# Optimization experiments

Measured on AMD Instinct MI355X. Metric: run time of the kernel, lower is better.

Reference implementation:

```python
import jax, jax.numpy as jnp
import numpy as np

NUM_HEADS = 16


def setup_inputs() -> dict:
    key = jax.random.key(0)
    ks = jax.random.split(key, 5)
    B, S, D = 2, 2048, 1024
    scale = 0.02
    return {
        "x": jax.random.normal(ks[0], (B, S, D), dtype=jnp.float32),
        "Wq": jax.random.normal(ks[1], (D, D), dtype=jnp.float32) * scale,
        "Wk": jax.random.normal(ks[2], (D, D), dtype=jnp.float32) * scale,
        "Wv": jax.random.normal(ks[3], (D, D), dtype=jnp.float32) * scale,
        "Wo": jax.random.normal(ks[4], (D, D), dtype=jnp.float32) * scale,
        "bo": jnp.zeros((D,), dtype=jnp.float32),
    }


def reference(x, Wq, Wk, Wv, Wo, bo):
    B, S, D = x.shape
    H = NUM_HEADS
    Dh = D // H
    # project and split heads -> [B, H, S, Dh]
    q = (x @ Wq).reshape(B, S, H, Dh).transpose(0, 2, 1, 3)
    k = (x @ Wk).reshape(B, S, H, Dh).transpose(0, 2, 1, 3)
    v = (x @ Wv).reshape(B, S, H, Dh).transpose(0, 2, 1, 3)
    # full causal attention scores [B, H, S, S]
    scores = jnp.einsum("bhqd,bhkd->bhqk", q, k)
    causal_mask = jnp.triu(jnp.ones((S, S), dtype=bool), k=1)
    scores = jnp.where(causal_mask, -jnp.inf, scores)
    attn = jax.nn.softmax(scores / jnp.sqrt(jnp.float32(Dh)), axis=-1)
    ctx = jnp.einsum("bhqk,bhkd->bhqd", attn, v)
    ctx = ctx.transpose(0, 2, 1, 3).reshape(B, S, D)
    return ctx @ Wo + bo
```

## Files before the change

kernel.cpp:

```cpp
#include <hip/hip_runtime.h>
#include <hip/hip_bf16.h>
#include <math.h>

typedef __bf16 bf16_t;
typedef bf16_t bf16x4 __attribute__((ext_vector_type(4)));
typedef bf16_t bf16x8 __attribute__((ext_vector_type(8)));
typedef float f32x4 __attribute__((ext_vector_type(4)));

#define MFMA16(a, b, c) __builtin_amdgcn_mfma_f32_16x16x32_bf16(a, b, c, 0, 0, 0)
#define NEG_BIG (-1e30f)
#define QSCALE 0.18033688f

#define GLL16(gp, lp)                                                          \
    __builtin_amdgcn_global_load_lds(                                          \
        (const __attribute__((address_space(1))) unsigned int*)(gp),           \
        (__attribute__((address_space(3))) unsigned int*)(lp), 16, 0, 0)


__global__ __launch_bounds__(256) void prep(const float* __restrict__ x,
                                            const float* __restrict__ Wq,
                                            const float* __restrict__ Wk,
                                            const float* __restrict__ Wv,
                                            const float* __restrict__ Wo,
                                            bf16_t* __restrict__ Xb,
                                            bf16_t* __restrict__ WTqkv,
                                            bf16_t* __restrict__ WoT) {
    __shared__ float tile[32][33];
    const int z = blockIdx.z;
    const int tx = threadIdx.x, ty = threadIdx.y;
    if (z == 4) {
        int i0 = (((blockIdx.y * 32 + blockIdx.x) * 256) + ty * 32 + tx) * 4;
        for (int j = 0; j < 4; j++) {
            int i = i0 + j * 1048576;
            float4 v = *(const float4*)(x + i);
            Xb[i + 0] = (bf16_t)v.x;
            Xb[i + 1] = (bf16_t)v.y;
            Xb[i + 2] = (bf16_t)v.z;
            Xb[i + 3] = (bf16_t)v.w;
        }
    } else {
        const float* W = (z == 0) ? Wq : (z == 1) ? Wk : (z == 2) ? Wv : Wo;
        bf16_t* WT = (z < 3) ? (WTqkv + (size_t)z * 1048576) : WoT;
        int bx = blockIdx.x * 32, by = blockIdx.y * 32;
        for (int i = 0; i < 32; i += 8)
            tile[ty + i][tx] = W[(size_t)(by + ty + i) * 1024 + bx + tx];
        __syncthreads();
        for (int i = 0; i < 32; i += 8)
            WT[(size_t)(bx + ty + i) * 1024 + by + tx] = (bf16_t)tile[tx][ty + i];
    }
}

__global__ __launch_bounds__(256) void gemm_qkv(const bf16_t* __restrict__ X,
                                                const bf16_t* __restrict__ WT,
                                                bf16_t* __restrict__ Qd,
                                                bf16_t* __restrict__ Kd,
                                                bf16_t* __restrict__ Vd) {
    __shared__ bf16_t AsmF[128 * 64];
    __shared__ bf16_t BsmF[128 * 64];
    const int which = blockIdx.z;
    const bf16_t* Wt = WT + (size_t)which * 1024 * 1024;
    const int bm = blockIdx.y * 128;
    const int bn = blockIdx.x * 128;
    const int tid = threadIdx.x;
    const int wave = tid >> 6, lane = tid & 63;
    const int wm = (wave >> 1) * 64, wn = (wave & 1) * 64;
    const int col = lane & 15, quad = lane >> 4;
    const int cswz = col & 7;
    const int lr8 = lane >> 3;
    const int jg = (lane & 7) ^ lr8;

    const int srow = wave * 32 + lr8;
    const bf16_t* gA = X  + (size_t)(bm + srow) * 1024 + jg * 8;
    const bf16_t* gB = Wt + (size_t)(bn + srow) * 1024 + jg * 8;
    bf16_t* lA = AsmF + wave * 2048;
    bf16_t* lB = BsmF + wave * 2048;

    f32x4 acc[4][4] = {};

    for (int k0 = 0; k0 < 1024; k0 += 64) {
        for (int j = 0; j < 4; j++) {
            GLL16(gA + (size_t)j * 8192 + k0, lA + j * 512);
            GLL16(gB + (size_t)j * 8192 + k0, lB + j * 512);
        }
        __syncthreads();
        for (int ks = 0; ks < 2; ks++) {
            bf16x8 af[4], bfr[4];
            for (int mi = 0; mi < 4; mi++)
                af[mi] = *(const bf16x8*)&AsmF[(wm + mi * 16 + col) * 64 +
                                               (((ks << 2) + quad) ^ cswz) * 8];
            for (int ni = 0; ni < 4; ni++)
                bfr[ni] = *(const bf16x8*)&BsmF[(wn + ni * 16 + col) * 64 +
                                                (((ks << 2) + quad) ^ cswz) * 8];
            if (which != 2) {
                for (int mi = 0; mi < 4; mi++)
                    for (int ni = 0; ni < 4; ni++)
                        acc[mi][ni] = MFMA16(af[mi], bfr[ni], acc[mi][ni]);
            } else {
                for (int mi = 0; mi < 4; mi++)
                    for (int ni = 0; ni < 4; ni++)
                        acc[mi][ni] = MFMA16(bfr[ni], af[mi], acc[mi][ni]);
            }
        }
        __syncthreads();
    }

    if (which != 2) {
        const float sc = (which == 0) ? QSCALE : 1.0f;
        for (int mi = 0; mi < 4; mi++) {
            for (int ni = 0; ni < 4; ni++) {
                int mbase = bm + wm + mi * 16 + quad * 4;
                int n = bn + wn + ni * 16 + col;
                int h = n >> 6, dh = n & 63;
                for (int r = 0; r < 4; r++) {
                    int m = mbase + r;
                    int b = m >> 11, s = m & 2047;
                    size_t bh = (size_t)b * 16 + h;
                    bf16_t val = (bf16_t)(acc[mi][ni][r] * sc);
                    if (which == 0) Qd[(bh * 2048 + s) * 64 + dh] = val;
                    else            Kd[(bh * 2048 + s) * 64 + dh] = val;
                }
            }
        }
    } else {
        for (int mi = 0; mi < 4; mi++) {
            for (int ni = 0; ni < 4; ni++) {
                int nbase = bn + wn + ni * 16 + quad * 4;
                int m = bm + wm + mi * 16 + col;
                int b = m >> 11, s = m & 2047;
                for (int r = 0; r < 4; r++) {
                    int n = nbase + r;
                    int h = n >> 6, dh = n & 63;
                    size_t bh = (size_t)b * 16 + h;
                    Vd[(bh * 64 + dh) * 2048 + s] = (bf16_t)acc[mi][ni][r];
                }
            }
        }
    }
}

__global__ __launch_bounds__(256) void attn(const bf16_t* __restrict__ Q,
                                            const bf16_t* __restrict__ K,
                                            const bf16_t* __restrict__ VT,
                                            bf16_t* __restrict__ CTX) {
    __shared__ bf16_t KsF[2 * 64 * 64];
    __shared__ bf16_t VsF[2 * 64 * 64];
    __shared__ bf16_t PsF[4 * 16 * 64];

    const int bidx = blockIdx.x;
    const int bh = bidx & 31;
    const int qt = 31 - (bidx >> 5);
    const int tid = threadIdx.x;
    const int wave = tid >> 6, lane = tid & 63;
    const int col = lane & 15, quad = lane >> 4;
    const int cswz = col & 7;
    const int lr8 = lane >> 3;
    const int jg = (lane & 7) ^ lr8;

    const bf16_t* Qb = Q + (size_t)bh * 2048 * 64;
    const bf16_t* Kb = K + (size_t)bh * 2048 * 64;
    const bf16_t* Vb = VT + (size_t)bh * 64 * 2048;

    const int strow = wave * 16 + lr8;
    const bf16_t* gK = Kb + (size_t)strow * 64 + jg * 8;
    const bf16_t* gV = Vb + (size_t)strow * 2048 + jg * 8;

    const int b_ = bh >> 4, h_ = bh & 15;

    bf16x8 ones;
    for (int i = 0; i < 8; i++) ones[i] = (bf16_t)1.0f;

    bf16_t* PsRow = PsF + wave * 1024 + col * 64;

    auto stage = [&](int k0, int bsel) {
        bf16_t* lK = KsF + bsel * 4096 + wave * 1024;
        bf16_t* lV = VsF + bsel * 4096 + wave * 1024;
        for (int j = 0; j < 2; j++) {
            GLL16(gK + (size_t)(k0 + j * 8) * 64, lK + j * 512);
            GLL16(gV + (size_t)(k0 + j * 8 * 2048), lV + j * 512);
        }
    };

    stage(0, 0);

    const int q0 = qt * 64;
    const int qrow = q0 + wave * 16 + col;
    const bf16x8 qf0 = *(const bf16x8*)&Qb[(size_t)qrow * 64 + quad * 8];
    const bf16x8 qf1 = *(const bf16x8*)&Qb[(size_t)qrow * 64 + 32 + quad * 8];

    f32x4 o[4] = {};
    f32x4 accl = {};

    const int nt = qt + 1;
    for (int g = 0; g < nt; g++) {
        __syncthreads();
        if (g + 1 < nt) stage((g + 1) * 64, (g + 1) & 1);

        const int bsel = g & 1;
        const bf16_t* Kbuf = KsF + bsel * 4096;
        const bf16_t* Vbuf = VsF + bsel * 4096;
        const bool diag = (g == qt);

        for (int ksub = 0; ksub < 4; ksub++) {
            bf16x8 a0 = *(const bf16x8*)&Kbuf[(ksub * 16 + col) * 64 +
                                              (quad ^ cswz) * 8];
            bf16x8 a1 = *(const bf16x8*)&Kbuf[(ksub * 16 + col) * 64 +
                                              ((4 + quad) ^ cswz) * 8];
            f32x4 z = {};
            z = MFMA16(a0, qf0, z);
            z = MFMA16(a1, qf1, z);
            if (diag) {
                for (int r = 0; r < 4; r++) {
                    int lk = ksub * 16 + quad * 4 + r;
                    if (lk > wave * 16 + col) z[r] = NEG_BIG;
                }
            }
            bf16x4 pw;
            for (int r = 0; r < 4; r++)
                pw[r] = (bf16_t)exp2f(z[r]);
            *(bf16x4*)&PsRow[((ksub * 2 + (quad >> 1)) ^ cswz) * 8 +
                             (quad & 1) * 4] = pw;
        }

        for (int ck = 0; ck < 2; ck++) {
            bf16x8 pf = *(const bf16x8*)&PsRow[((ck * 4 + quad) ^ cswz) * 8];
            accl = MFMA16(pf, ones, accl);
            for (int d = 0; d < 4; d++) {
                bf16x8 vf = *(const bf16x8*)&Vbuf[(d * 16 + col) * 64 +
                                                  (((ck << 2) + quad) ^ cswz) * 8];
                o[d] = MFMA16(pf, vf, o[d]);
            }
        }
    }

    for (int d = 0; d < 4; d++) {
        for (int r = 0; r < 4; r++) {
            int s = q0 + wave * 16 + quad * 4 + r;
            CTX[((size_t)(b_ * 2048 + s)) * 1024 + h_ * 64 + d * 16 + col] =
                (bf16_t)(o[d][r] / fmaxf(accl[r], 1e-20f));
        }
    }
}

__global__ __launch_bounds__(256) void gemm_out(const bf16_t* __restrict__ X,
                                                const bf16_t* __restrict__ WT,
                                                const float* __restrict__ BO,
                                                float* __restrict__ OUT) {
    __shared__ bf16_t AsmF[64 * 64];
    __shared__ bf16_t BsmF[128 * 64];
    const int bm = blockIdx.y * 64;
    const int bn = blockIdx.x * 128;
    const int tid = threadIdx.x;
    const int wave = tid >> 6, lane = tid & 63;
    const int wm = (wave >> 1) * 32, wn = (wave & 1) * 64;
    const int col = lane & 15, quad = lane >> 4;
    const int cswz = col & 7;
    const int lr8 = lane >> 3;
    const int jg = (lane & 7) ^ lr8;

    const int arow = wave * 16 + lr8;
    const int brow = wave * 32 + lr8;
    const bf16_t* gA = X  + (size_t)(bm + arow) * 1024 + jg * 8;
    const bf16_t* gB = WT + (size_t)(bn + brow) * 1024 + jg * 8;
    bf16_t* lA = AsmF + wave * 1024;
    bf16_t* lB = BsmF + wave * 2048;

    f32x4 acc[2][4] = {};

    for (int k0 = 0; k0 < 1024; k0 += 64) {
        for (int j = 0; j < 2; j++)
            GLL16(gA + (size_t)j * 8192 + k0, lA + j * 512);
        for (int j = 0; j < 4; j++)
            GLL16(gB + (size_t)j * 8192 + k0, lB + j * 512);
        __syncthreads();
        for (int ks = 0; ks < 2; ks++) {
            bf16x8 af[2], bfr[4];
            for (int mi = 0; mi < 2; mi++)
                af[mi] = *(const bf16x8*)&AsmF[(wm + mi * 16 + col) * 64 +
                                               (((ks << 2) + quad) ^ cswz) * 8];
            for (int ni = 0; ni < 4; ni++)
                bfr[ni] = *(const bf16x8*)&BsmF[(wn + ni * 16 + col) * 64 +
                                                (((ks << 2) + quad) ^ cswz) * 8];
            for (int mi = 0; mi < 2; mi++)
                for (int ni = 0; ni < 4; ni++)
                    acc[mi][ni] = MFMA16(af[mi], bfr[ni], acc[mi][ni]);
        }
        __syncthreads();
    }

    for (int mi = 0; mi < 2; mi++) {
        for (int ni = 0; ni < 4; ni++) {
            int mbase = bm + wm + mi * 16 + quad * 4;
            int n = bn + wn + ni * 16 + col;
            float bov = BO[n];
            for (int r = 0; r < 4; r++) {
                int m = mbase + r;
                OUT[(size_t)m * 1024 + n] = acc[mi][ni][r] + bov;
            }
        }
    }
}

extern "C" void kernel_launch(void* const* d_in, const int* in_sizes, int n_in,
                              void* d_out, int out_size, void* d_ws, size_t ws_size,
                              hipStream_t stream) {
    const float* x  = (const float*)d_in[0];
    const float* Wq = (const float*)d_in[1];
    const float* Wk = (const float*)d_in[2];
    const float* Wv = (const float*)d_in[3];
    const float* Wo = (const float*)d_in[4];
    const float* bo = (const float*)d_in[5];
    float* out = (float*)d_out;

    const size_t MEG = 1048576;
    bf16_t* base  = (bf16_t*)d_ws;
    bf16_t* Xb    = base;
    bf16_t* WTqkv = base + 4 * MEG;
    bf16_t* WoT   = base + 7 * MEG;
    bf16_t* Qb    = base + 8 * MEG;
    bf16_t* Kb    = base + 12 * MEG;
    bf16_t* Vb    = base + 16 * MEG;
    bf16_t* Cb    = base + 20 * MEG;

    prep<<<dim3(32, 32, 5), dim3(32, 8), 0, stream>>>(x, Wq, Wk, Wv, Wo,
                                                      Xb, WTqkv, WoT);
    gemm_qkv<<<dim3(8, 32, 3), 256, 0, stream>>>(Xb, WTqkv, Qb, Kb, Vb);
    attn<<<1024, 256, 0, stream>>>(Qb, Kb, Vb, Cb);
    gemm_out<<<dim3(8, 64), 256, 0, stream>>>(Cb, WoT, bo, out);
}
```

Measured before the change: 181.6 us.

## Double-buffer LDS tiles in QKV and output projection GEMMs

Both projection GEMMs now use two LDS buffers per operand. The next K-tile is prefetched with global_load_lds right after the barrier, while MFMAs run on the current tile. This removes one of the two __syncthreads per iteration and is meant to hide global-load latency behind compute. The cost is double the LDS per block, which may lower the number of blocks resident per CU.

```diff
diff --git a/kernel.cpp b/kernel.cpp
--- a/kernel.cpp
+++ b/kernel.cpp
@@ -55,8 +55,8 @@
                                                 bf16_t* __restrict__ Qd,
                                                 bf16_t* __restrict__ Kd,
                                                 bf16_t* __restrict__ Vd) {
-    __shared__ bf16_t AsmF[128 * 64];
-    __shared__ bf16_t BsmF[128 * 64];
+    __shared__ bf16_t AsmF[2 * 128 * 64];
+    __shared__ bf16_t BsmF[2 * 128 * 64];
     const int which = blockIdx.z;
     const bf16_t* Wt = WT + (size_t)which * 1024 * 1024;
     const int bm = blockIdx.y * 128;
@@ -72,24 +72,32 @@
     const int srow = wave * 32 + lr8;
     const bf16_t* gA = X  + (size_t)(bm + srow) * 1024 + jg * 8;
     const bf16_t* gB = Wt + (size_t)(bn + srow) * 1024 + jg * 8;
-    bf16_t* lA = AsmF + wave * 2048;
-    bf16_t* lB = BsmF + wave * 2048;
-
-    f32x4 acc[4][4] = {};
-
-    for (int k0 = 0; k0 < 1024; k0 += 64) {
+
+    auto stage = [&](int k0, int bsel) {
+        bf16_t* lA = AsmF + bsel * 8192 + wave * 2048;
+        bf16_t* lB = BsmF + bsel * 8192 + wave * 2048;
         for (int j = 0; j < 4; j++) {
             GLL16(gA + (size_t)j * 8192 + k0, lA + j * 512);
             GLL16(gB + (size_t)j * 8192 + k0, lB + j * 512);
         }
+    };
+
+    f32x4 acc[4][4] = {};
+
+    stage(0, 0);
+    for (int kt = 0; kt < 16; kt++) {
         __syncthreads();
+        if (kt + 1 < 16) stage((kt + 1) * 64, (kt + 1) & 1);
+
+        const bf16_t* Abuf = AsmF + (kt & 1) * 8192;
+        const bf16_t* Bbuf = BsmF + (kt & 1) * 8192;
         for (int ks = 0; ks < 2; ks++) {
             bf16x8 af[4], bfr[4];
             for (int mi = 0; mi < 4; mi++)
-                af[mi] = *(const bf16x8*)&AsmF[(wm + mi * 16 + col) * 64 +
+                af[mi] = *(const bf16x8*)&Abuf[(wm + mi * 16 + col) * 64 +
                                                (((ks << 2) + quad) ^ cswz) * 8];
             for (int ni = 0; ni < 4; ni++)
-                bfr[ni] = *(const bf16x8*)&BsmF[(wn + ni * 16 + col) * 64 +
+                bfr[ni] = *(const bf16x8*)&Bbuf[(wn + ni * 16 + col) * 64 +
                                                 (((ks << 2) + quad) ^ cswz) * 8];
             if (which != 2) {
                 for (int mi = 0; mi < 4; mi++)
@@ -101,7 +109,6 @@
                         acc[mi][ni] = MFMA16(bfr[ni], af[mi], acc[mi][ni]);
             }
         }
-        __syncthreads();
     }
 
     if (which != 2) {
@@ -245,8 +252,8 @@
                                                 const bf16_t* __restrict__ WT,
                                                 const float* __restrict__ BO,
                                                 float* __restrict__ OUT) {
-    __shared__ bf16_t AsmF[64 * 64];
-    __shared__ bf16_t BsmF[128 * 64];
+    __shared__ bf16_t AsmF[2 * 64 * 64];
+    __shared__ bf16_t BsmF[2 * 128 * 64];
     const int bm = blockIdx.y * 64;
     const int bn = blockIdx.x * 128;
     const int tid = threadIdx.x;
@@ -261,30 +268,37 @@
     const int brow = wave * 32 + lr8;
     const bf16_t* gA = X  + (size_t)(bm + arow) * 1024 + jg * 8;
     const bf16_t* gB = WT + (size_t)(bn + brow) * 1024 + jg * 8;
-    bf16_t* lA = AsmF + wave * 1024;
-    bf16_t* lB = BsmF + wave * 2048;
-
-    f32x4 acc[2][4] = {};
-
-    for (int k0 = 0; k0 < 1024; k0 += 64) {
+
+    auto stage = [&](int k0, int bsel) {
+        bf16_t* lA = AsmF + bsel * 4096 + wave * 1024;
+        bf16_t* lB = BsmF + bsel * 8192 + wave * 2048;
         for (int j = 0; j < 2; j++)
             GLL16(gA + (size_t)j * 8192 + k0, lA + j * 512);
         for (int j = 0; j < 4; j++)
             GLL16(gB + (size_t)j * 8192 + k0, lB + j * 512);
+    };
+
+    f32x4 acc[2][4] = {};
+
+    stage(0, 0);
+    for (int kt = 0; kt < 16; kt++) {
         __syncthreads();
+        if (kt + 1 < 16) stage((kt + 1) * 64, (kt + 1) & 1);
+
+        const bf16_t* Abuf = AsmF + (kt & 1) * 4096;
+        const bf16_t* Bbuf = BsmF + (kt & 1) * 8192;
         for (int ks = 0; ks < 2; ks++) {
             bf16x8 af[2], bfr[4];
             for (int mi = 0; mi < 2; mi++)
-                af[mi] = *(const bf16x8*)&AsmF[(wm + mi * 16 + col) * 64 +
+                af[mi] = *(const bf16x8*)&Abuf[(wm + mi * 16 + col) * 64 +
                                                (((ks << 2) + quad) ^ cswz) * 8];
             for (int ni = 0; ni < 4; ni++)
-                bfr[ni] = *(const bf16x8*)&BsmF[(wn + ni * 16 + col) * 64 +
+                bfr[ni] = *(const bf16x8*)&Bbuf[(wn + ni * 16 + col) * 64 +
                                                 (((ks << 2) + quad) ^ cswz) * 8];
             for (int mi = 0; mi < 2; mi++)
                 for (int ni = 0; ni < 4; ni++)
                     acc[mi][ni] = MFMA16(af[mi], bfr[ni], acc[mi][ni]);
         }
-        __syncthreads();
     }
 
     for (int mi = 0; mi < 2; mi++) {
```

After: 185.3 us. 2.0% more time.
